# Kernel optimization log

Measured on AMD Instinct MI355X. Metric: run time of the kernel, lower is better.

## Reference

```python
import jax, jax.numpy as jnp
import numpy as np

DIM = 1024
N_HEADS = 16
HEAD_DIM = DIM // N_HEADS
SCALE = HEAD_DIM ** -0.5


def setup_inputs() -> dict:
    key = jax.random.key(0)
    ks = jax.random.split(key, 5)
    x = jax.random.normal(ks[0], (4, 2048, DIM), dtype=jnp.float32)
    # nn.Linear weights stored as [out, in]; we keep [in, out] for x @ W
    w_qkv = jax.random.normal(ks[1], (DIM, 3 * DIM), dtype=jnp.float32) * (DIM ** -0.5)
    b_qkv = jnp.zeros((3 * DIM,), dtype=jnp.float32)
    w_proj = jax.random.normal(ks[2], (DIM, DIM), dtype=jnp.float32) * (DIM ** -0.5)
    b_proj = jnp.zeros((DIM,), dtype=jnp.float32)
    return {"x": x, "w_qkv": w_qkv, "b_qkv": b_qkv, "w_proj": w_proj, "b_proj": b_proj}


def reference(x, w_qkv, b_qkv, w_proj, b_proj):
    B, S, D = x.shape
    qkv = x @ w_qkv + b_qkv                                   # [B,S,3D]
    qkv = qkv.reshape(B, S, 3, N_HEADS, HEAD_DIM)
    qkv = jnp.transpose(qkv, (2, 0, 3, 1, 4))                 # [3,B,H,S,hd]
    q, k, v = qkv[0], qkv[1], qkv[2]
    attn = jnp.einsum("bhqd,bhkd->bhqk", q, k) * SCALE        # [B,H,S,S]
    attn = jax.nn.softmax(attn, axis=-1)
    out = jnp.einsum("bhqk,bhkd->bhqd", attn, v)              # [B,H,S,hd]
    out = jnp.transpose(out, (0, 2, 1, 3)).reshape(B, S, D)   # [B,S,D]
    return out @ w_proj + b_proj
```

## Files before the change

kernel.cpp:

```cpp
#include <hip/hip_runtime.h>
#include <hip/hip_bf16.h>

typedef float f32x4 __attribute__((ext_vector_type(4)));
typedef short bf16x8 __attribute__((ext_vector_type(8)));
typedef unsigned short ushort8 __attribute__((ext_vector_type(8)));

__device__ __forceinline__ unsigned short f2bf(float f) {
    union { float f; unsigned u; } v; v.f = f;
    unsigned r = v.u + 0x7fffu + ((v.u >> 16) & 1u);
    return (unsigned short)(r >> 16);
}

__device__ __forceinline__ unsigned short f2bf_hw(float f) {
    union { __hip_bfloat16 b; unsigned short u; } cv;
    cv.b = __float2bfloat16(f);
    return cv.u;
}

#define GLDS16(g, l)                                                        \
    __builtin_amdgcn_global_load_lds(                                       \
        (const __attribute__((address_space(1))) unsigned int*)(const void*)(g), \
        (__attribute__((address_space(3))) unsigned int*)(void*)(l), 16, 0, 0)

__global__ __launch_bounds__(256) void k_cvt(const float* __restrict__ in,
                                             unsigned short* __restrict__ out, int n8) {
    int i = blockIdx.x * 256 + threadIdx.x;
    if (i >= n8) return;
    float4 a = ((const float4*)in)[i * 2];
    float4 b = ((const float4*)in)[i * 2 + 1];
    ushort8 o = { f2bf(a.x), f2bf(a.y), f2bf(a.z), f2bf(a.w),
                  f2bf(b.x), f2bf(b.y), f2bf(b.z), f2bf(b.w) };
    ((ushort8*)out)[i] = o;
}

__global__ __launch_bounds__(256) void k_tpose(const float* __restrict__ in,
                                               unsigned short* __restrict__ out,
                                               int R, int C) {
    __shared__ float t[32][33];
    int c0 = blockIdx.x * 32, r0 = blockIdx.y * 32;
    int tx = threadIdx.x, ty = threadIdx.y;
#pragma unroll
    for (int i = 0; i < 4; i++)
        t[ty + i * 8][tx] = in[(size_t)(r0 + ty + i * 8) * C + c0 + tx];
    __syncthreads();
#pragma unroll
    for (int i = 0; i < 4; i++)
        out[(size_t)(c0 + ty + i * 8) * R + r0 + tx] = f2bf(t[tx][ty + i * 8]);
}

template <int MODE>
__global__ __launch_bounds__(256)
void k_gemm(const unsigned short* __restrict__ A, const unsigned short* __restrict__ Bt,
            const float* __restrict__ bias, int M, int N, int K,
            float* __restrict__ outF, unsigned short* __restrict__ q_ws,
            unsigned short* __restrict__ k_ws, unsigned short* __restrict__ vt_ws) {
    __shared__ __attribute__((aligned(16))) unsigned short Ash[128 * 32];
    __shared__ __attribute__((aligned(16))) unsigned short Bsh[128 * 32];
    int tid = threadIdx.x;
    int lane = tid & 63, w = tid >> 6;
    int wr = w >> 1, wc = w & 1;
    int m0 = blockIdx.y * 128, n0 = blockIdx.x * 128;
    f32x4 acc[4][4] = {};

    int srow = tid >> 2, sk = (tid & 3) * 8;
    const unsigned short* aS0 = A + (size_t)(m0 + srow) * K + sk;
    const unsigned short* aS1 = A + (size_t)(m0 + 64 + srow) * K + sk;
    const unsigned short* bS0 = Bt + (size_t)(n0 + srow) * K + sk;
    const unsigned short* bS1 = Bt + (size_t)(n0 + 64 + srow) * K + sk;
    unsigned short* aD0 = Ash + w * 512;
    unsigned short* aD1 = Ash + 2048 + w * 512;
    unsigned short* bD0 = Bsh + w * 512;
    unsigned short* bD1 = Bsh + 2048 + w * 512;

    int ko = (lane >> 4) * 8;
    int arow = (wr * 64 + (lane & 15)) * 32;
    int brow = (wc * 64 + (lane & 15)) * 32;

    for (int k0 = 0; k0 < K; k0 += 32) {
        GLDS16(aS0, aD0);
        GLDS16(aS1, aD1);
        GLDS16(bS0, bD0);
        GLDS16(bS1, bD1);
        aS0 += 32; aS1 += 32; bS0 += 32; bS1 += 32;
        __syncthreads();
        bf16x8 af[4], bfr[4];
#pragma unroll
        for (int i = 0; i < 4; i++) {
            af[i]  = *(const bf16x8*)&Ash[arow + i * 16 * 32 + ko];
            bfr[i] = *(const bf16x8*)&Bsh[brow + i * 16 * 32 + ko];
        }
#pragma unroll
        for (int i = 0; i < 4; i++)
#pragma unroll
            for (int j = 0; j < 4; j++)
                acc[i][j] = __builtin_amdgcn_mfma_f32_16x16x32_bf16(af[i], bfr[j], acc[i][j], 0, 0, 0);
        __syncthreads();
    }

    int colBase = n0 + wc * 64 + (lane & 15);
    int rowBase = m0 + wr * 64 + ((lane >> 4) << 2);
#pragma unroll
    for (int i = 0; i < 4; i++)
#pragma unroll
        for (int j = 0; j < 4; j++)
#pragma unroll
            for (int r = 0; r < 4; r++) {
                int m = rowBase + i * 16 + r;
                int n = colBase + j * 16;
                float v = acc[i][j][r] + bias[n];
                if constexpr (MODE == 0) {
                    outF[(size_t)m * N + n] = v;
                } else {
                    int which = n >> 10, rem = n & 1023;
                    int h = rem >> 6, d = rem & 63;
                    int b = m >> 11, s = m & 2047;
                    int bh = b * 16 + h;
                    if (which == 0)
                        q_ws[((size_t)bh * 2048 + s) * 64 + d] = f2bf(v * 0.125f);
                    else if (which == 1)
                        k_ws[((size_t)bh * 2048 + s) * 64 + d] = f2bf(v);
                    else
                        vt_ws[((size_t)bh * 64 + d) * 2048 + s] = f2bf(v);
                }
            }
}

__global__ __launch_bounds__(256)
void k_attn(const unsigned short* __restrict__ q_ws, const unsigned short* __restrict__ k_ws,
            const unsigned short* __restrict__ vt_ws, unsigned short* __restrict__ o_ws) {
    __shared__ __attribute__((aligned(16))) unsigned short Ksh[2][64 * 64];
    __shared__ __attribute__((aligned(16))) unsigned short Vsh[2][64 * 64];
    __shared__ __attribute__((aligned(16))) unsigned short Psh[128 * 72];
    int tid = threadIdx.x, lane = tid & 63, w = tid >> 6;
    int l15 = lane & 15, g = lane >> 4;
    int bh = blockIdx.y, b = bh >> 4, h = bh & 15;
    int q0 = blockIdx.x * 128;
    const unsigned short* qp = q_ws + (size_t)bh * 2048 * 64;
    const unsigned short* kp = k_ws + (size_t)bh * 2048 * 64;
    const unsigned short* vp = vt_ws + (size_t)bh * 64 * 2048;

    int ko = g * 8;
    bf16x8 qf[2][2];
#pragma unroll
    for (int half = 0; half < 2; half++) {
        const unsigned short* qr = qp + (size_t)(q0 + w * 32 + half * 16 + l15) * 64;
        qf[half][0] = *(const bf16x8*)(qr + ko);
        qf[half][1] = *(const bf16x8*)(qr + 32 + ko);
    }

    f32x4 oacc[2][4] = {};
    float lacc[2][4] = {};

    int srow = tid >> 2, squad = tid & 3;
    int ssw = (srow & 7) << 3;
    int sbase = srow * 64;
    int sc0 = (squad * 16) ^ ssw;
    int sc1 = (squad * 16 + 8) ^ ssw;

    const unsigned short* kNext = kp + (size_t)srow * 64 + squad * 16;
    const unsigned short* vNext = vp + (size_t)srow * 2048 + squad * 16;

    uint4 kr0, kr1, vr0, vr1;
#define LOADT()                                                                \
    {                                                                          \
        kr0 = *(const uint4*)kNext; kr1 = *(const uint4*)(kNext + 8);          \
        vr0 = *(const uint4*)vNext; vr1 = *(const uint4*)(vNext + 8);          \
        kNext += 64 * 64; vNext += 64;                                         \
    }
#define STORET(BUF)                                                            \
    {                                                                          \
        *(uint4*)&Ksh[BUF][sbase + sc0] = kr0;                                 \
        *(uint4*)&Ksh[BUF][sbase + sc1] = kr1;                                 \
        *(uint4*)&Vsh[BUF][sbase + sc0] = vr0;                                 \
        *(uint4*)&Vsh[BUF][sbase + sc1] = vr1;                                 \
    }

    LOADT();
    STORET(0);
    __syncthreads();

    for (int t = 0; t < 32; t++) {
        int cur = t & 1;
        if (t < 31) LOADT();

        f32x4 s[2][4];
        __builtin_amdgcn_s_setprio(1);
#pragma unroll
        for (int ct = 0; ct < 4; ct++) {
            int krow = ct * 16 + l15;
            int ksw = (krow & 7) << 3;
            const unsigned short* kb = &Ksh[cur][krow * 64];
            bf16x8 kb0 = *(const bf16x8*)&kb[ko ^ ksw];
            bf16x8 kb1 = *(const bf16x8*)&kb[(32 + ko) ^ ksw];
#pragma unroll
            for (int half = 0; half < 2; half++) {
                f32x4 sa = {};
                sa = __builtin_amdgcn_mfma_f32_16x16x32_bf16(qf[half][0], kb0, sa, 0, 0, 0);
                sa = __builtin_amdgcn_mfma_f32_16x16x32_bf16(qf[half][1], kb1, sa, 0, 0, 0);
                s[half][ct] = sa;
            }
        }
        __builtin_amdgcn_s_setprio(0);

#pragma unroll
        for (int half = 0; half < 2; half++)
#pragma unroll
            for (int r = 0; r < 4; r++) {
                int prow = (w * 32 + half * 16 + 4 * g + r) * 72;
#pragma unroll
                for (int ct = 0; ct < 4; ct++) {
                    float p = __expf(s[half][ct][r]);
                    lacc[half][r] += p;
                    Psh[prow + ct * 16 + l15] = f2bf_hw(p);
                }
            }

        __syncthreads();

        bf16x8 pa[2][2];
#pragma unroll
        for (int half = 0; half < 2; half++) {
            int parow = (w * 32 + half * 16 + l15) * 72;
            pa[half][0] = *(const bf16x8*)&Psh[parow + ko];
            pa[half][1] = *(const bf16x8*)&Psh[parow + 32 + ko];
        }
        __builtin_amdgcn_s_setprio(1);
#pragma unroll
        for (int ct = 0; ct < 4; ct++) {
            int vrow = ct * 16 + l15;
            int vsw = (vrow & 7) << 3;
            const unsigned short* vb = &Vsh[cur][vrow * 64];
            bf16x8 vb0 = *(const bf16x8*)&vb[ko ^ vsw];
            bf16x8 vb1 = *(const bf16x8*)&vb[(32 + ko) ^ vsw];
#pragma unroll
            for (int half = 0; half < 2; half++) {
                oacc[half][ct] = __builtin_amdgcn_mfma_f32_16x16x32_bf16(pa[half][0], vb0, oacc[half][ct], 0, 0, 0);
                oacc[half][ct] = __builtin_amdgcn_mfma_f32_16x16x32_bf16(pa[half][1], vb1, oacc[half][ct], 0, 0, 0);
            }
        }
        __builtin_amdgcn_s_setprio(0);

        if (t < 31) STORET(cur ^ 1);
        __syncthreads();
    }
#undef LOADT
#undef STORET

#pragma unroll
    for (int half = 0; half < 2; half++)
#pragma unroll
        for (int r = 0; r < 4; r++) {
            float lf = lacc[half][r];
#pragma unroll
            for (int off = 8; off; off >>= 1) lf += __shfl_xor(lf, off);
            float inv = 1.0f / lf;
            int srw = q0 + w * 32 + half * 16 + 4 * g + r;
#pragma unroll
            for (int ct = 0; ct < 4; ct++) {
                int d = ct * 16 + l15;
                o_ws[((size_t)(b * 2048 + srw) * 16 + h) * 64 + d] = f2bf_hw(oacc[half][ct][r] * inv);
            }
        }
}

extern "C" void kernel_launch(void* const* d_in, const int* in_sizes, int n_in,
                              void* d_out, int out_size, void* d_ws, size_t ws_size,
                              hipStream_t stream) {
    const float* x      = (const float*)d_in[0];
    const float* w_qkv  = (const float*)d_in[1];
    const float* b_qkv  = (const float*)d_in[2];
    const float* w_proj = (const float*)d_in[3];
    const float* b_proj = (const float*)d_in[4];
    float* out = (float*)d_out;

    char* ws = (char*)d_ws;
    unsigned short* xb  = (unsigned short*)(ws);
    unsigned short* wqt = (unsigned short*)(ws + 16777216);
    unsigned short* wpt = (unsigned short*)(ws + 23068672);
    unsigned short* qw  = (unsigned short*)(ws + 25165824);
    unsigned short* kw  = (unsigned short*)(ws + 41943040);
    unsigned short* vtw = (unsigned short*)(ws + 58720256);
    unsigned short* ow  = (unsigned short*)(ws + 75497472);

    k_cvt<<<4096, 256, 0, stream>>>(x, xb, 1048576);
    k_tpose<<<dim3(96, 32), dim3(32, 8), 0, stream>>>(w_qkv, wqt, 1024, 3072);
    k_tpose<<<dim3(32, 32), dim3(32, 8), 0, stream>>>(w_proj, wpt, 1024, 1024);
    k_gemm<1><<<dim3(24, 64), 256, 0, stream>>>(xb, wqt, b_qkv, 8192, 3072, 1024,
                                                nullptr, qw, kw, vtw);
    k_attn<<<dim3(16, 64), 256, 0, stream>>>(qw, kw, vtw, ow);
    k_gemm<0><<<dim3(8, 64), 256, 0, stream>>>(ow, wpt, b_proj, 8192, 1024, 1024,
                                               out, nullptr, nullptr, nullptr);
}
```

Measured before the change: 251.1 us.

## Remap workgroups for XCD locality and stage V transpose through LDS

Workgroup IDs in both the GEMM and attention kernels are remapped so that consecutive tiles land on the same XCD, which should improve L2 reuse of shared A/B rows and K/V heads on the chiplet GPU. In the QKV GEMM, V tiles are now transposed through a padded LDS buffer and written as contiguous 16-byte vector stores instead of strided scalar stores. This adds LDS use and a sync for V blocks, and the remap assumes the grid size is divisible by 8.

```diff
diff --git a/kernel.cpp b/kernel.cpp
--- a/kernel.cpp
+++ b/kernel.cpp
@@ -56,10 +56,17 @@
             unsigned short* __restrict__ k_ws, unsigned short* __restrict__ vt_ws) {
     __shared__ __attribute__((aligned(16))) unsigned short Ash[128 * 32];
     __shared__ __attribute__((aligned(16))) unsigned short Bsh[128 * 32];
+    __shared__ __attribute__((aligned(16))) unsigned short Vt[(MODE == 1) ? 128 * 136 : 8];
     int tid = threadIdx.x;
     int lane = tid & 63, w = tid >> 6;
     int wr = w >> 1, wc = w & 1;
-    int m0 = blockIdx.y * 128, n0 = blockIdx.x * 128;
+
+    int nbx = gridDim.x;
+    int flat = blockIdx.y * nbx + blockIdx.x;
+    int cpx = (nbx * gridDim.y) >> 3;
+    int wg = (flat & 7) * cpx + (flat >> 3);
+    int m0 = (wg / nbx) * 128, n0 = (wg % nbx) * 128;
+
     f32x4 acc[4][4] = {};
 
     int srow = tid >> 2, sk = (tid & 3) * 8;
@@ -99,6 +106,33 @@
 
     int colBase = n0 + wc * 64 + (lane & 15);
     int rowBase = m0 + wr * 64 + ((lane >> 4) << 2);
+
+    if constexpr (MODE == 1) {
+        if (n0 >= 2048) {
+#pragma unroll
+            for (int i = 0; i < 4; i++)
+#pragma unroll
+                for (int j = 0; j < 4; j++)
+#pragma unroll
+                    for (int r = 0; r < 4; r++) {
+                        int nl = wc * 64 + j * 16 + (lane & 15);
+                        int ml = wr * 64 + i * 16 + ((lane >> 4) << 2) + r;
+                        Vt[nl * 136 + ml] = f2bf(acc[i][j][r] + bias[n0 + nl]);
+                    }
+            __syncthreads();
+            int row = tid >> 1, col0 = (tid & 1) * 64;
+            int rem = (n0 + row) & 1023;
+            unsigned short* dst = vt_ws
+                + ((size_t)((m0 >> 11) * 16 + (rem >> 6)) * 64 + (rem & 63)) * 2048
+                + (m0 & 2047) + col0;
+            const unsigned short* src = &Vt[row * 136 + col0];
+#pragma unroll
+            for (int q2 = 0; q2 < 8; q2++)
+                ((uint4*)dst)[q2] = ((const uint4*)src)[q2];
+            return;
+        }
+    }
+
 #pragma unroll
     for (int i = 0; i < 4; i++)
 #pragma unroll
@@ -117,10 +151,8 @@
                     int bh = b * 16 + h;
                     if (which == 0)
                         q_ws[((size_t)bh * 2048 + s) * 64 + d] = f2bf(v * 0.125f);
-                    else if (which == 1)
+                    else
                         k_ws[((size_t)bh * 2048 + s) * 64 + d] = f2bf(v);
-                    else
-                        vt_ws[((size_t)bh * 64 + d) * 2048 + s] = f2bf(v);
                 }
             }
 }
@@ -133,8 +165,13 @@
     __shared__ __attribute__((aligned(16))) unsigned short Psh[128 * 72];
     int tid = threadIdx.x, lane = tid & 63, w = tid >> 6;
     int l15 = lane & 15, g = lane >> 4;
-    int bh = blockIdx.y, b = bh >> 4, h = bh & 15;
-    int q0 = blockIdx.x * 128;
+
+    int flat = blockIdx.y * 16 + blockIdx.x;
+    int wg = (flat & 7) * 128 + (flat >> 3);
+    int bh = wg >> 4;
+    int q0 = (wg & 15) * 128;
+    int b = bh >> 4, h = bh & 15;
+
     const unsigned short* qp = q_ws + (size_t)bh * 2048 * 64;
     const unsigned short* kp = k_ws + (size_t)bh * 2048 * 64;
     const unsigned short* vp = vt_ws + (size_t)bh * 64 * 2048;
```

Measured after the change: 241.9 us. 1.04x faster.
